# Performance work log

Measured on AMD Instinct MI355X. Metric: run time of the kernel, lower is better.

Reference implementation:

```python
import jax, jax.numpy as jnp
import numpy as np

B, C, H, W = 4, 512, 64, 64
IC = C // 2  # inter_plane
EPS = 1e-5


def _conv1x1(x, w, b=None):
    # x: [b,c,h,w], w: [o,c] -> [b,o,h,w]
    y = jnp.einsum('bchw,oc->bohw', x, w)
    if b is not None:
        y = y + b[None, :, None, None]
    return y


def setup_inputs() -> dict:
    key = jax.random.key(0)
    ks = jax.random.split(key, 20)
    rn = lambda i, sh, s=0.02: jax.random.normal(ks[i], sh, jnp.float32) * s
    return {
        'xA': jax.random.normal(ks[0], (B, C, H, W), jnp.float32),
        'wk': rn(1, (IC, C)), 'bk': rn(2, (IC,)),
        'wv': rn(3, (IC, C)), 'bv': rn(4, (IC,)),
        'wq': rn(5, (IC, C)), 'bq': rn(6, (IC,)),
        'wwg': rn(7, (IC, IC)),
        'bn1_g': jnp.ones((IC,), jnp.float32), 'bn1_b': rn(8, (IC,)),
        'bn1_m': rn(9, (IC,)), 'bn1_v': jax.random.uniform(ks[10], (IC,), jnp.float32, 0.5, 1.5),
        'wout': rn(11, (C, IC)), 'bout': rn(12, (C,)),
        'bn2_g': jnp.ones((C,), jnp.float32), 'bn2_b': rn(13, (C,)),
        'bn2_m': rn(14, (C,)), 'bn2_v': jax.random.uniform(ks[15], (C,), jnp.float32, 0.5, 1.5),
    }


def reference(xA, wk, bk, wv, bv, wq, bq, wwg, bn1_g, bn1_b, bn1_m, bn1_v,
              wout, bout, bn2_g, bn2_b, bn2_m, bn2_v):
    b, c, h, w = xA.shape
    n = h * w
    k = _conv1x1(xA, wk, bk).reshape(b, IC, n)   # [b,ic,n]
    v = _conv1x1(xA, wv, bv).reshape(b, IC, n)   # [b,ic,n] (permuted via einsum below)
    q = _conv1x1(xA, wq, bq).reshape(b, IC, n)   # [b,ic,n]
    # AV = softmax(v^T @ q, axis=2): [b,n,n]
    attn = jax.nn.softmax(jnp.einsum('bcn,bcm->bnm', v, q), axis=2)
    av = jnp.einsum('bcn,bnm->bcm', k, attn)     # [b,ic,n]
    # conv1d 1x1 (no bias) + BatchNorm1d (eval mode)
    avw = jnp.einsum('oc,bcn->bon', wwg, av)
    scale1 = bn1_g / jnp.sqrt(bn1_v + EPS)
    avw = (avw - bn1_m[None, :, None]) * scale1[None, :, None] + bn1_b[None, :, None]
    avw = avw.reshape(b, IC, h, w)
    # out conv + BatchNorm2d (eval) + residual + relu
    o = _conv1x1(avw, wout, bout)
    scale2 = bn2_g / jnp.sqrt(bn2_v + EPS)
    o = (o - bn2_m[None, :, None, None]) * scale2[None, :, None, None] + bn2_b[None, :, None, None]
    return jax.nn.relu(o + xA)
```

## Files before the change

kernel.cpp:

```cpp
#include <hip/hip_runtime.h>


#define N_ 4096
#define C_ 512
#define IC_ 256
#define B_ 4

typedef __bf16 bf16_t;
typedef __bf16 bf16x8 __attribute__((ext_vector_type(8)));
typedef __bf16 bf16x4 __attribute__((ext_vector_type(4)));
typedef float f32x4 __attribute__((ext_vector_type(4)));

#define GLD(g, l) __builtin_amdgcn_global_load_lds(                              \
    (const __attribute__((address_space(1))) void*)(g),                          \
    (__attribute__((address_space(3))) void*)(l), 16, 0, 0)

__device__ __forceinline__ void gemm_bt_128x128(
    const bf16_t* __restrict__ A, int lda,
    const bf16_t* __restrict__ Bt, int ldb,
    int K, int kt0, int m0, int n0,
    bf16_t* lsA, bf16_t* lsB, f32x4 acc[4][4])
{
    const int tid  = threadIdx.x;
    const int wave = tid >> 6, lane = tid & 63;
    const int wr = (wave >> 1) * 64, wc = (wave & 1) * 64;
    const int q = lane >> 4, l15 = lane & 15;
    const int srow = lane >> 3;
    const int scol = (((lane & 7) ^ (srow & 7)) * 8);
    const int swz  = l15 & 7;

    for (int kt = kt0; kt < kt0 + K; kt += 64) {
#pragma unroll
        for (int c = 0; c < 4; ++c) {
            const int ch = wave * 4 + c;
            GLD(A  + (size_t)(m0 + ch * 8 + srow) * lda + kt + scol, lsA + ch * 512);
            GLD(Bt + (size_t)(n0 + ch * 8 + srow) * ldb + kt + scol, lsB + ch * 512);
        }
        __syncthreads();
#pragma unroll
        for (int ks = 0; ks < 2; ++ks) {
            bf16x8 af[4], bfr[4];
            const int co = ((ks * 4 + q) ^ swz) * 8;
#pragma unroll
            for (int i = 0; i < 4; ++i) {
                af[i]  = *(const bf16x8*)&lsA[(wr + i * 16 + l15) * 64 + co];
                bfr[i] = *(const bf16x8*)&lsB[(wc + i * 16 + l15) * 64 + co];
            }
#pragma unroll
            for (int i = 0; i < 4; ++i)
#pragma unroll
                for (int j = 0; j < 4; ++j)
                    acc[i][j] = __builtin_amdgcn_mfma_f32_16x16x32_bf16(
                        af[i], bfr[j], acc[i][j], 0, 0, 0);
        }
        __syncthreads();
    }
}

#define ACC_ZERO(acc)                                                           \
    _Pragma("unroll") for (int i = 0; i < 4; ++i)                               \
    _Pragma("unroll") for (int j = 0; j < 4; ++j)                               \
        acc[i][j] = f32x4{0.f, 0.f, 0.f, 0.f};

__global__ __launch_bounds__(256) void castw3_k(
    const float* __restrict__ wk, const float* __restrict__ wv,
    const float* __restrict__ wq, bf16_t* __restrict__ Wb3)
{
    const int i = blockIdx.x * 256 + threadIdx.x;
    float v;
    if      (i < 131072) v = wk[i];
    else if (i < 262144) v = wv[i - 131072];
    else                 v = wq[i - 262144];
    Wb3[i] = (bf16_t)v;
}

__global__ __launch_bounds__(256) void wf_k(
    const float* __restrict__ wwg, const float* __restrict__ wout,
    const float* __restrict__ bout,
    const float* __restrict__ g1, const float* __restrict__ b1,
    const float* __restrict__ m1, const float* __restrict__ v1,
    const float* __restrict__ g2, const float* __restrict__ b2,
    const float* __restrict__ m2, const float* __restrict__ v2,
    bf16_t* __restrict__ Wfb, float* __restrict__ bfv)
{
    const int o = blockIdx.x;
    const int j = threadIdx.x;
    __shared__ float ws[256];
    __shared__ float red[4];

    const float s1 = g1[j] * rsqrtf(v1[j] + 1e-5f);
    const float wo = wout[o * 256 + j];
    ws[j] = wo * s1;
    float bp = wo * (b1[j] - m1[j] * s1);
#pragma unroll
    for (int off = 32; off > 0; off >>= 1) bp += __shfl_down(bp, off);
    if ((j & 63) == 0) red[j >> 6] = bp;
    __syncthreads();

    float acc = 0.f;
#pragma unroll 4
    for (int ic = 0; ic < 256; ++ic)
        acc += ws[ic] * wwg[ic * 256 + j];

    const float s2 = g2[o] * rsqrtf(v2[o] + 1e-5f);
    Wfb[o * 256 + j] = (bf16_t)(acc * s2);
    if (j == 0)
        bfv[o] = s2 * (red[0] + red[1] + red[2] + red[3] + bout[o])
                 - s2 * m2[o] + b2[o];
}

__global__ __launch_bounds__(256) void txa_k(
    const float* __restrict__ xA, bf16_t* __restrict__ xAt)
{
    __shared__ float t[32][33];
    const int b = blockIdx.z;
    const int n0 = blockIdx.x * 32, c0 = blockIdx.y * 32;
    const int tx = threadIdx.x, ty = threadIdx.y;
    const float* X = xA + (size_t)b * C_ * N_;
    bf16_t* Y = xAt + (size_t)b * N_ * C_;
#pragma unroll
    for (int r = 0; r < 4; ++r)
        t[ty + r * 8][tx] = X[(size_t)(c0 + ty + r * 8) * N_ + n0 + tx];
    __syncthreads();
#pragma unroll
    for (int r = 0; r < 4; ++r)
        Y[(size_t)(n0 + ty + r * 8) * C_ + c0 + tx] = (bf16_t)t[tx][ty + r * 8];
}

__global__ __launch_bounds__(256) void conv_mfma_k(
    const bf16_t* __restrict__ Wb3,
    const float* __restrict__ bk, const float* __restrict__ bv,
    const float* __restrict__ bq, const bf16_t* __restrict__ xAt,
    bf16_t* __restrict__ Kb, bf16_t* __restrict__ Vt, bf16_t* __restrict__ Qt)
{
    __shared__ bf16_t smem[16384];
    const int which = blockIdx.z % 3, b = blockIdx.z / 3;
    const bf16_t* A = Wb3 + which * 131072;
    const float* bias = (which == 0) ? bk : (which == 1 ? bv : bq);
    const bf16_t* Bt = xAt + (size_t)b * N_ * C_;
    const int n0 = blockIdx.x * 128, m0 = blockIdx.y * 128;

    f32x4 acc[4][4];
    ACC_ZERO(acc);
    gemm_bt_128x128(A, C_, Bt, C_, C_, 0, m0, n0, smem, smem + 8192, acc);

    const int lane = threadIdx.x & 63, wave = threadIdx.x >> 6;
    const int q = lane >> 4, l15 = lane & 15;
    const int wr = (wave >> 1) * 64, wc = (wave & 1) * 64;

    if (which == 0) {
        bf16_t* Y = Kb + (size_t)b * IC_ * N_;
#pragma unroll
        for (int i = 0; i < 4; ++i)
#pragma unroll
            for (int r = 0; r < 4; ++r) {
                const int o = m0 + wr + i * 16 + q * 4 + r;
                const float bo = bias[o];
#pragma unroll
                for (int j = 0; j < 4; ++j)
                    Y[(size_t)o * N_ + n0 + wc + j * 16 + l15] =
                        (bf16_t)(acc[i][j][r] + bo);
            }
    } else {
        bf16_t* Y = ((which == 1) ? Vt : Qt) + (size_t)b * N_ * IC_;
#pragma unroll
        for (int i = 0; i < 4; ++i) {
            const int ob = m0 + wr + i * 16 + q * 4;
            float bo[4];
#pragma unroll
            for (int r = 0; r < 4; ++r) bo[r] = bias[ob + r];
#pragma unroll
            for (int j = 0; j < 4; ++j) {
                const int n = n0 + wc + j * 16 + l15;
                bf16x4 v4;
#pragma unroll
                for (int r = 0; r < 4; ++r) v4[r] = (bf16_t)(acc[i][j][r] + bo[r]);
                *(bf16x4*)&Y[(size_t)n * IC_ + ob] = v4;
            }
        }
    }
}

__global__ __launch_bounds__(256) void s_mfma_t_k(
    const bf16_t* __restrict__ Qt, const bf16_t* __restrict__ Vt,
    bf16_t* __restrict__ Pt, float* __restrict__ rowsum)
{
    __shared__ bf16_t smem[17408];
    const int b  = blockIdx.z;
    const int n0 = blockIdx.x * 128;
    const int m0 = blockIdx.y * 128;
    const size_t NIC = (size_t)N_ * IC_;
    const bf16_t* Qb = Qt + (size_t)b * NIC;
    const bf16_t* Vb = Vt + (size_t)b * NIC;
    bf16_t* Pb = Pt + (size_t)b * N_ * N_;
    float* rs = rowsum + b * N_;

    f32x4 acc[4][4];
    ACC_ZERO(acc);
    gemm_bt_128x128(Qb, IC_, Vb, IC_, IC_, 0, m0, n0, smem, smem + 8192, acc);

    const int tid = threadIdx.x;
    const int lane = tid & 63, wave = tid >> 6;
    const int q = lane >> 4, l15 = lane & 15;
    const int wr = (wave >> 1) * 64, wc = (wave & 1) * 64;

#pragma unroll
    for (int j = 0; j < 4; ++j) {
        float cs = 0.f;
#pragma unroll
        for (int i = 0; i < 4; ++i)
#pragma unroll
            for (int r = 0; r < 4; ++r) {
                const float e = __expf(acc[i][j][r]);
                cs += e;
                smem[(wr + i * 16 + q * 4 + r) * 136 + wc + j * 16 + l15] = (bf16_t)e;
            }
        cs += __shfl_xor(cs, 16);
        cs += __shfl_xor(cs, 32);
        if (q == 0) atomicAdd(&rs[n0 + wc + j * 16 + l15], cs);
    }
    __syncthreads();

    const int rr = tid >> 4;
    const int cc = (tid & 15) * 8;
#pragma unroll
    for (int p = 0; p < 8; ++p) {
        const int mm = rr + p * 16;
        const bf16x8 v = *(const bf16x8*)&smem[mm * 136 + cc];
        *(bf16x8*)&Pb[(size_t)(m0 + mm) * N_ + n0 + cc] = v;
    }
}

__global__ __launch_bounds__(256) void kscale_k(
    bf16_t* __restrict__ Kb, const float* __restrict__ rowsum)
{
    const size_t i8 = ((size_t)blockIdx.x * 256 + threadIdx.x) * 8;
    const int n = (int)(i8 & (N_ - 1));
    const int b = (int)(i8 >> 20);
    const float* rs = rowsum + b * N_;
    bf16x8 v = *(bf16x8*)&Kb[i8];
    const f32x4 r0 = *(const f32x4*)&rs[n];
    const f32x4 r1 = *(const f32x4*)&rs[n + 4];
#pragma unroll
    for (int k = 0; k < 4; ++k) {
        v[k]     = (bf16_t)((float)v[k]     / r0[k]);
        v[4 + k] = (bf16_t)((float)v[4 + k] / r1[k]);
    }
    *(bf16x8*)&Kb[i8] = v;
}

__global__ __launch_bounds__(256) void av_mfma_k(
    const bf16_t* __restrict__ Pt, const bf16_t* __restrict__ Kb,
    float* __restrict__ avPart)
{
    __shared__ bf16_t smem[16384];
    const int m0 = blockIdx.x * 128;
    const int c0 = blockIdx.y * 128;
    const int b  = blockIdx.z >> 1;
    const int z  = blockIdx.z & 1;
    const size_t NIC = (size_t)N_ * IC_;

    f32x4 acc[4][4];
    ACC_ZERO(acc);
    gemm_bt_128x128(Pt + (size_t)b * N_ * N_, N_, Kb + (size_t)b * NIC, N_,
                    2048, z * 2048, m0, c0, smem, smem + 8192, acc);

    const int lane = threadIdx.x & 63, wave = threadIdx.x >> 6;
    const int q = lane >> 4, l15 = lane & 15;
    const int wr = (wave >> 1) * 64, wc = (wave & 1) * 64;
    float* Y = avPart + ((size_t)z * B_ + b) * NIC;

#pragma unroll
    for (int i = 0; i < 4; ++i)
#pragma unroll
        for (int r = 0; r < 4; ++r) {
            const int m = m0 + wr + i * 16 + q * 4 + r;
#pragma unroll
            for (int j = 0; j < 4; ++j)
                Y[(size_t)m * IC_ + c0 + wc + j * 16 + l15] = acc[i][j][r];
        }
}

__global__ __launch_bounds__(256) void avred_k(
    const float* __restrict__ avPart, bf16_t* __restrict__ avTb)
{
    const size_t i8 = ((size_t)blockIdx.x * 256 + threadIdx.x) * 8;
    const float* base = avPart + i8;
    f32x4 s0 = *(const f32x4*)&base[0];
    f32x4 s1 = *(const f32x4*)&base[4];
    s0 += *(const f32x4*)&base[4194304];
    s1 += *(const f32x4*)&base[4194304 + 4];
    bf16x8 o;
#pragma unroll
    for (int k = 0; k < 4; ++k) { o[k] = (bf16_t)s0[k]; o[4 + k] = (bf16_t)s1[k]; }
    *(bf16x8*)&avTb[i8] = o;
}

__global__ __launch_bounds__(256) void out_mfma_k(
    const bf16_t* __restrict__ Wfb, const float* __restrict__ bfv,
    const bf16_t* __restrict__ avTb,
    const float* __restrict__ xA, float* __restrict__ out)
{
    __shared__ bf16_t smem[16384];
    const int b = blockIdx.z;
    const bf16_t* Bt = avTb + (size_t)b * N_ * IC_;
    const int n0 = blockIdx.x * 128, o0 = blockIdx.y * 128;

    f32x4 acc[4][4];
    ACC_ZERO(acc);
    gemm_bt_128x128(Wfb, IC_, Bt, IC_, IC_, 0, o0, n0, smem, smem + 8192, acc);

    const int lane = threadIdx.x & 63, wave = threadIdx.x >> 6;
    const int q = lane >> 4, l15 = lane & 15;
    const int wr = (wave >> 1) * 64, wc = (wave & 1) * 64;

#pragma unroll
    for (int i = 0; i < 4; ++i)
#pragma unroll
        for (int r = 0; r < 4; ++r) {
            const int o = o0 + wr + i * 16 + q * 4 + r;
            const float bo = bfv[o];
#pragma unroll
            for (int j = 0; j < 4; ++j) {
                const int n = n0 + wc + j * 16 + l15;
                const size_t idx = ((size_t)b * C_ + o) * N_ + n;
                out[idx] = fmaxf(acc[i][j][r] + bo + xA[idx], 0.f);
            }
        }
}

extern "C" void kernel_launch(void* const* d_in, const int* in_sizes, int n_in,
                              void* d_out, int out_size, void* d_ws, size_t ws_size,
                              hipStream_t stream)
{
    const float* xA    = (const float*)d_in[0];
    const float* wk    = (const float*)d_in[1];
    const float* bk    = (const float*)d_in[2];
    const float* wv    = (const float*)d_in[3];
    const float* bv    = (const float*)d_in[4];
    const float* wq    = (const float*)d_in[5];
    const float* bq    = (const float*)d_in[6];
    const float* wwg   = (const float*)d_in[7];
    const float* bn1_g = (const float*)d_in[8];
    const float* bn1_b = (const float*)d_in[9];
    const float* bn1_m = (const float*)d_in[10];
    const float* bn1_v = (const float*)d_in[11];
    const float* wout  = (const float*)d_in[12];
    const float* bout  = (const float*)d_in[13];
    const float* bn2_g = (const float*)d_in[14];
    const float* bn2_b = (const float*)d_in[15];
    const float* bn2_m = (const float*)d_in[16];
    const float* bn2_v = (const float*)d_in[17];
    float* out = (float*)d_out;

    char* p = (char*)d_ws;
    bf16_t* Wb3    = (bf16_t*)p; p += 786432;
    bf16_t* Wfb    = (bf16_t*)p; p += 262144;
    float*  bfv    = (float*)p;  p += 2048;
    bf16_t* xAt    = (bf16_t*)p;
    bf16_t* avTb   = (bf16_t*)p; p += 16777216;
    bf16_t* Kb     = (bf16_t*)p; p += 8388608;
    bf16_t* Vt     = (bf16_t*)p; p += 8388608;
    bf16_t* Qt     = (bf16_t*)p; p += 8388608;
    float*  rowsum = (float*)p;  p += 65536;
    bf16_t* Pt     = (bf16_t*)p; p += 134217728;
    float*  avPart = (float*)p;  p += 33554432;

    castw3_k<<<1536, 256, 0, stream>>>(wk, wv, wq, Wb3);
    wf_k<<<512, 256, 0, stream>>>(wwg, wout, bout, bn1_g, bn1_b, bn1_m, bn1_v,
                                  bn2_g, bn2_b, bn2_m, bn2_v, Wfb, bfv);
    (void)hipMemsetAsync(rowsum, 0, 65536, stream);
    txa_k<<<dim3(N_ / 32, C_ / 32, B_), dim3(32, 8), 0, stream>>>(xA, xAt);
    conv_mfma_k<<<dim3(N_ / 128, IC_ / 128, 3 * B_), 256, 0, stream>>>(
        Wb3, bk, bv, bq, xAt, Kb, Vt, Qt);

    s_mfma_t_k<<<dim3(N_ / 128, N_ / 128, B_), 256, 0, stream>>>(
        Qt, Vt, Pt, rowsum);
    kscale_k<<<2048, 256, 0, stream>>>(Kb, rowsum);
    av_mfma_k<<<dim3(N_ / 128, IC_ / 128, 2 * B_), 256, 0, stream>>>(
        Pt, Kb, avPart);
    avred_k<<<2048, 256, 0, stream>>>(avPart, avTb);

    out_mfma_k<<<dim3(N_ / 128, C_ / 128, B_), 256, 0, stream>>>(
        Wfb, bfv, avTb, xA, out);
}
```

Before: 326.8 us.

## Retile AV GEMM to 64x256 full-K tiles and fuse prep kernels

The AV GEMM changes from 128x128 tiles with a split-K of two, plus a separate fp32 reduction kernel, to 64-row tiles that cover all 256 output channels and the full K. Each P tile is now read once instead of twice, and the fp32 partial write/read round trip is gone, since the bf16 output is written through a shared-memory staging buffer. The weight-cast, folded-weight and rowsum-zeroing launches are merged into one prep kernel to cut launch count. The cost is fewer blocks for the AV GEMM (256 total) and a longer serial K loop per block with no double buffering, which may hurt occupancy and latency hiding.

```diff
diff --git a/kernel.cpp b/kernel.cpp
--- a/kernel.cpp
+++ b/kernel.cpp
@@ -62,51 +62,54 @@
     _Pragma("unroll") for (int j = 0; j < 4; ++j)                               \
         acc[i][j] = f32x4{0.f, 0.f, 0.f, 0.f};
 
-__global__ __launch_bounds__(256) void castw3_k(
+__global__ __launch_bounds__(256) void prep_k(
     const float* __restrict__ wk, const float* __restrict__ wv,
-    const float* __restrict__ wq, bf16_t* __restrict__ Wb3)
-{
-    const int i = blockIdx.x * 256 + threadIdx.x;
-    float v;
-    if      (i < 131072) v = wk[i];
-    else if (i < 262144) v = wv[i - 131072];
-    else                 v = wq[i - 262144];
-    Wb3[i] = (bf16_t)v;
-}
-
-__global__ __launch_bounds__(256) void wf_k(
+    const float* __restrict__ wq,
     const float* __restrict__ wwg, const float* __restrict__ wout,
     const float* __restrict__ bout,
     const float* __restrict__ g1, const float* __restrict__ b1,
     const float* __restrict__ m1, const float* __restrict__ v1,
     const float* __restrict__ g2, const float* __restrict__ b2,
     const float* __restrict__ m2, const float* __restrict__ v2,
-    bf16_t* __restrict__ Wfb, float* __restrict__ bfv)
-{
-    const int o = blockIdx.x;
-    const int j = threadIdx.x;
+    bf16_t* __restrict__ Wb3, bf16_t* __restrict__ Wfb,
+    float* __restrict__ bfv, float* __restrict__ rowsum)
+{
+    const int bid = blockIdx.x;
     __shared__ float ws[256];
     __shared__ float red[4];
 
-    const float s1 = g1[j] * rsqrtf(v1[j] + 1e-5f);
-    const float wo = wout[o * 256 + j];
-    ws[j] = wo * s1;
-    float bp = wo * (b1[j] - m1[j] * s1);
-#pragma unroll
-    for (int off = 32; off > 0; off >>= 1) bp += __shfl_down(bp, off);
-    if ((j & 63) == 0) red[j >> 6] = bp;
-    __syncthreads();
-
-    float acc = 0.f;
+    if (bid < 1536) {
+        const int i = bid * 256 + threadIdx.x;
+        float v;
+        if      (i < 131072) v = wk[i];
+        else if (i < 262144) v = wv[i - 131072];
+        else                 v = wq[i - 262144];
+        Wb3[i] = (bf16_t)v;
+    } else if (bid < 2048) {
+        const int o = bid - 1536;
+        const int j = threadIdx.x;
+        const float s1 = g1[j] * rsqrtf(v1[j] + 1e-5f);
+        const float wo = wout[o * 256 + j];
+        ws[j] = wo * s1;
+        float bp = wo * (b1[j] - m1[j] * s1);
+#pragma unroll
+        for (int off = 32; off > 0; off >>= 1) bp += __shfl_down(bp, off);
+        if ((j & 63) == 0) red[j >> 6] = bp;
+        __syncthreads();
+
+        float acc = 0.f;
 #pragma unroll 4
-    for (int ic = 0; ic < 256; ++ic)
-        acc += ws[ic] * wwg[ic * 256 + j];
-
-    const float s2 = g2[o] * rsqrtf(v2[o] + 1e-5f);
-    Wfb[o * 256 + j] = (bf16_t)(acc * s2);
-    if (j == 0)
-        bfv[o] = s2 * (red[0] + red[1] + red[2] + red[3] + bout[o])
-                 - s2 * m2[o] + b2[o];
+        for (int ic = 0; ic < 256; ++ic)
+            acc += ws[ic] * wwg[ic * 256 + j];
+
+        const float s2 = g2[o] * rsqrtf(v2[o] + 1e-5f);
+        Wfb[o * 256 + j] = (bf16_t)(acc * s2);
+        if (j == 0)
+            bfv[o] = s2 * (red[0] + red[1] + red[2] + red[3] + bout[o])
+                     - s2 * m2[o] + b2[o];
+    } else {
+        rowsum[(bid - 2048) * 256 + threadIdx.x] = 0.f;
+    }
 }
 
 __global__ __launch_bounds__(256) void txa_k(
@@ -251,49 +254,77 @@
 
 __global__ __launch_bounds__(256) void av_mfma_k(
     const bf16_t* __restrict__ Pt, const bf16_t* __restrict__ Kb,
-    float* __restrict__ avPart)
-{
-    __shared__ bf16_t smem[16384];
-    const int m0 = blockIdx.x * 128;
-    const int c0 = blockIdx.y * 128;
-    const int b  = blockIdx.z >> 1;
-    const int z  = blockIdx.z & 1;
+    bf16_t* __restrict__ avTb)
+{
+    __shared__ bf16_t smem[20480];
+    bf16_t* lsA = smem;
+    bf16_t* lsB = smem + 4096;
+    const int b  = blockIdx.y;
+    const int m0 = blockIdx.x * 64;
     const size_t NIC = (size_t)N_ * IC_;
+    const bf16_t* Pb  = Pt + (size_t)b * N_ * N_ + (size_t)m0 * N_;
+    const bf16_t* Kbb = Kb + (size_t)b * NIC;
+
+    const int tid = threadIdx.x;
+    const int wave = tid >> 6, lane = tid & 63;
+    const int q = lane >> 4, l15 = lane & 15;
+    const int srow = lane >> 3;
+    const int scol = (((lane & 7) ^ (srow & 7)) * 8);
+    const int swz  = l15 & 7;
 
     f32x4 acc[4][4];
     ACC_ZERO(acc);
-    gemm_bt_128x128(Pt + (size_t)b * N_ * N_, N_, Kb + (size_t)b * NIC, N_,
-                    2048, z * 2048, m0, c0, smem, smem + 8192, acc);
-
-    const int lane = threadIdx.x & 63, wave = threadIdx.x >> 6;
-    const int q = lane >> 4, l15 = lane & 15;
-    const int wr = (wave >> 1) * 64, wc = (wave & 1) * 64;
-    float* Y = avPart + ((size_t)z * B_ + b) * NIC;
+
+    for (int kt = 0; kt < N_; kt += 64) {
+#pragma unroll
+        for (int c = 0; c < 2; ++c) {
+            const int ch = wave * 2 + c;
+            GLD(Pb + (size_t)(ch * 8 + srow) * N_ + kt + scol, lsA + ch * 512);
+        }
+#pragma unroll
+        for (int c = 0; c < 8; ++c) {
+            const int ch = wave * 8 + c;
+            GLD(Kbb + (size_t)(ch * 8 + srow) * N_ + kt + scol, lsB + ch * 512);
+        }
+        __syncthreads();
+#pragma unroll
+        for (int ks = 0; ks < 2; ++ks) {
+            const int co = ((ks * 4 + q) ^ swz) * 8;
+            bf16x8 af[4], bfr[4];
+#pragma unroll
+            for (int i = 0; i < 4; ++i) {
+                af[i]  = *(const bf16x8*)&lsA[(i * 16 + l15) * 64 + co];
+                bfr[i] = *(const bf16x8*)&lsB[(wave * 64 + i * 16 + l15) * 64 + co];
+            }
+#pragma unroll
+            for (int i = 0; i < 4; ++i)
+#pragma unroll
+                for (int j = 0; j < 4; ++j)
+                    acc[i][j] = __builtin_amdgcn_mfma_f32_16x16x32_bf16(
+                        af[i], bfr[j], acc[i][j], 0, 0, 0);
+        }
+        __syncthreads();
+    }
 
 #pragma unroll
     for (int i = 0; i < 4; ++i)
 #pragma unroll
-        for (int r = 0; r < 4; ++r) {
-            const int m = m0 + wr + i * 16 + q * 4 + r;
-#pragma unroll
-            for (int j = 0; j < 4; ++j)
-                Y[(size_t)m * IC_ + c0 + wc + j * 16 + l15] = acc[i][j][r];
-        }
-}
-
-__global__ __launch_bounds__(256) void avred_k(
-    const float* __restrict__ avPart, bf16_t* __restrict__ avTb)
-{
-    const size_t i8 = ((size_t)blockIdx.x * 256 + threadIdx.x) * 8;
-    const float* base = avPart + i8;
-    f32x4 s0 = *(const f32x4*)&base[0];
-    f32x4 s1 = *(const f32x4*)&base[4];
-    s0 += *(const f32x4*)&base[4194304];
-    s1 += *(const f32x4*)&base[4194304 + 4];
-    bf16x8 o;
-#pragma unroll
-    for (int k = 0; k < 4; ++k) { o[k] = (bf16_t)s0[k]; o[4 + k] = (bf16_t)s1[k]; }
-    *(bf16x8*)&avTb[i8] = o;
+        for (int j = 0; j < 4; ++j)
+#pragma unroll
+            for (int r = 0; r < 4; ++r)
+                smem[(i * 16 + q * 4 + r) * 264 + wave * 64 + j * 16 + l15] =
+                    (bf16_t)acc[i][j][r];
+    __syncthreads();
+
+    bf16_t* Y = avTb + (size_t)b * NIC + (size_t)m0 * IC_;
+    const int erow = tid >> 2;
+    const int ecol = (tid & 3) * 8;
+#pragma unroll
+    for (int p = 0; p < 8; ++p) {
+        const int col = ecol + p * 32;
+        const bf16x8 v = *(const bf16x8*)&smem[erow * 264 + col];
+        *(bf16x8*)&Y[(size_t)erow * IC_ + col] = v;
+    }
 }
 
 __global__ __launch_bounds__(256) void out_mfma_k(
@@ -364,12 +395,11 @@
     bf16_t* Qt     = (bf16_t*)p; p += 8388608;
     float*  rowsum = (float*)p;  p += 65536;
     bf16_t* Pt     = (bf16_t*)p; p += 134217728;
-    float*  avPart = (float*)p;  p += 33554432;
-
-    castw3_k<<<1536, 256, 0, stream>>>(wk, wv, wq, Wb3);
-    wf_k<<<512, 256, 0, stream>>>(wwg, wout, bout, bn1_g, bn1_b, bn1_m, bn1_v,
-                                  bn2_g, bn2_b, bn2_m, bn2_v, Wfb, bfv);
-    (void)hipMemsetAsync(rowsum, 0, 65536, stream);
+
+    prep_k<<<2112, 256, 0, stream>>>(wk, wv, wq, wwg, wout, bout,
+                                     bn1_g, bn1_b, bn1_m, bn1_v,
+                                     bn2_g, bn2_b, bn2_m, bn2_v,
+                                     Wb3, Wfb, bfv, rowsum);
     txa_k<<<dim3(N_ / 32, C_ / 32, B_), dim3(32, 8), 0, stream>>>(xA, xAt);
     conv_mfma_k<<<dim3(N_ / 128, IC_ / 128, 3 * B_), 256, 0, stream>>>(
         Wb3, bk, bv, bq, xAt, Kb, Vt, Qt);
@@ -377,9 +407,7 @@
     s_mfma_t_k<<<dim3(N_ / 128, N_ / 128, B_), 256, 0, stream>>>(
         Qt, Vt, Pt, rowsum);
     kscale_k<<<2048, 256, 0, stream>>>(Kb, rowsum);
-    av_mfma_k<<<dim3(N_ / 128, IC_ / 128, 2 * B_), 256, 0, stream>>>(
-        Pt, Kb, avPart);
-    avred_k<<<2048, 256, 0, stream>>>(avPart, avTb);
+    av_mfma_k<<<dim3(N_ / 64, B_), 256, 0, stream>>>(Pt, Kb, avTb);
 
     out_mfma_k<<<dim3(N_ / 128, C_ / 128, B_), 256, 0, stream>>>(
         Wfb, bfv, avTb, xA, out);
```

New measurement: 330.9 us. About the same (+1.2%).
